# Kernel optimization log

Hardware: AMD Instinct MI355X
Metric: run time of the kernel (lower is better)

Reference implementation:

```python
import jax, jax.numpy as jnp
import numpy as np

B = 128      # graphs per side
N = 512      # nodes per graph (max for dense batch)
TOT = B * N  # 65536 total nodes per side
FIN = 128
F1, F2, F3 = 64, 64, 32
TN = 16      # tensor_neurons
BINS = 16
BN = 16      # bottleneck neurons
E = 16 * TOT # edges per side


def setup_inputs() -> dict:
    key = jax.random.key(0)
    ks = jax.random.split(key, 20)
    nrm = lambda k, shape, s=0.1: (jax.random.normal(k, shape, jnp.float32) * s)
    batch = jnp.repeat(jnp.arange(B, dtype=jnp.int32), N)
    return {
        'x1': jax.random.normal(ks[0], (TOT, FIN), jnp.float32),
        'x2': jax.random.normal(ks[1], (TOT, FIN), jnp.float32),
        'edge_index_1': jax.random.randint(ks[2], (2, E), 0, TOT, jnp.int32),
        'edge_index_2': jax.random.randint(ks[3], (2, E), 0, TOT, jnp.int32),
        'batch_1': batch,
        'batch_2': batch,
        'W1': nrm(ks[4], (FIN, F1)), 'b1': jnp.zeros((F1,), jnp.float32),
        'W2': nrm(ks[5], (F1, F2)), 'b2': jnp.zeros((F2,), jnp.float32),
        'W3': nrm(ks[6], (F2, F3)), 'b3': jnp.zeros((F3,), jnp.float32),
        'att_W': nrm(ks[7], (F3, F3)),
        'ntn_W': nrm(ks[8], (F3, F3, TN)),
        'ntn_V': nrm(ks[9], (TN, 2 * F3)),
        'ntn_b': jnp.zeros((TN,), jnp.float32),
        'fc1_W': nrm(ks[10], (TN + BINS, BN)),
        'fc1_b': jnp.zeros((BN,), jnp.float32),
        'sc_W': nrm(ks[11], (BN, 1)),
        'sc_b': jnp.zeros((1,), jnp.float32),
    }


def _gcn(x, W, b, src, dst):
    # PyG GCNConv: h = XW; add self-loops; D^{-1/2} A D^{-1/2} aggregation; + bias
    h = x @ W
    deg = jnp.zeros((TOT,), jnp.float32).at[dst].add(1.0) + 1.0  # incl. self-loop
    dis = jax.lax.rsqrt(deg)
    msg = h[src] * (dis[src] * dis[dst])[:, None]
    out = jnp.zeros_like(h).at[dst].add(msg) + h * (1.0 / deg)[:, None]
    return out + b


def _conv_pass(x, ei, W1, b1, W2, b2, W3, b3):
    # dropout is identity in eval mode
    h = jax.nn.relu(_gcn(x, W1, b1, ei[0], ei[1]))
    h = jax.nn.relu(_gcn(h, W2, b2, ei[0], ei[1]))
    return _gcn(h, W3, b3, ei[0], ei[1])


def _to_dense_batch(x, batch):
    ones = jnp.ones((TOT,), jnp.float32)
    cnt = jax.ops.segment_sum(ones, batch, num_segments=B)  # [B]
    starts = jnp.concatenate([jnp.zeros((1,), jnp.int32), jnp.cumsum(cnt.astype(jnp.int32))[:-1]])
    pos = jnp.arange(TOT, dtype=jnp.int32) - starts[batch]
    dense = jnp.zeros((B, N, x.shape[1]), x.dtype).at[batch, pos].set(x)
    cnt_i = cnt.astype(jnp.int32)
    return dense, cnt_i


def _histogram(af1, af2, batch_1, batch_2):
    d1, cnt1 = _to_dense_batch(af1, batch_1)
    d2, cnt2 = _to_dense_batch(af2, batch_2)
    nn = jnp.maximum(cnt1, cnt2)  # [B]
    sc = jax.nn.sigmoid(jax.lax.stop_gradient(jnp.einsum('bnf,bmf->bnm', d1, d2)))  # [B,N,N]
    ar = jnp.arange(N)
    valid = (ar[None, :, None] < nn[:, None, None]) & (ar[None, None, :] < nn[:, None, None])
    big = jnp.float32(1e30)
    mn = jnp.min(jnp.where(valid, sc, big), axis=(1, 2))
    mx = jnp.max(jnp.where(valid, sc, -big), axis=(1, 2))
    rng = jnp.where(mx > mn, mx - mn, jnp.float32(1.0))
    bidx = jnp.clip(jnp.floor((sc - mn[:, None, None]) / rng[:, None, None] * BINS), 0, BINS - 1).astype(jnp.int32)
    ids = jnp.arange(B, dtype=jnp.int32)[:, None, None] * BINS + bidx
    hist = jnp.zeros((B * BINS,), jnp.float32).at[ids.reshape(-1)].add(valid.reshape(-1).astype(jnp.float32))
    hist = hist.reshape(B, BINS)
    return hist / hist.sum(axis=1, keepdims=True)


def _att_pool(h, batch, att_W):
    cnt = jax.ops.segment_sum(jnp.ones((TOT,), jnp.float32), batch, num_segments=B)
    g = jax.ops.segment_sum(h @ att_W, batch, num_segments=B) / cnt[:, None]
    t = jnp.tanh(g)                                   # [B,F3] global context
    s = jax.nn.sigmoid(jnp.sum(h * t[batch], axis=1)) # [TOT] attention
    return jax.ops.segment_sum(h * s[:, None], batch, num_segments=B)


def reference(x1, x2, edge_index_1, edge_index_2, batch_1, batch_2,
              W1, b1, W2, b2, W3, b3, att_W, ntn_W, ntn_V, ntn_b,
              fc1_W, fc1_b, sc_W, sc_b):
    af1 = _conv_pass(x1, edge_index_1, W1, b1, W2, b2, W3, b3)
    af2 = _conv_pass(x2, edge_index_2, W1, b1, W2, b2, W3, b3)
    hist = _histogram(af1, af2, batch_1, batch_2)
    p1 = _att_pool(af1, batch_1, att_W)
    p2 = _att_pool(af2, batch_2, att_W)
    # Neural Tensor Network
    bilin = jnp.einsum('bi,ijk,bj->bk', p1, ntn_W, p2)
    blk = jnp.concatenate([p1, p2], axis=1) @ ntn_V.T
    scores = jax.nn.relu(bilin + blk + ntn_b)
    feat = jnp.concatenate([scores, hist], axis=1)
    h = jax.nn.relu(feat @ fc1_W + fc1_b)
    return jax.nn.sigmoid(h @ sc_W + sc_b).reshape(-1)
```

## Files before the change

### kernel.cpp

```cpp
#include <hip/hip_runtime.h>
#include <hip/hip_bf16.h>

constexpr int    TOT = 65536;
constexpr int    TOT2 = 131072;
constexpr long long Ec = 16LL * TOT;
constexpr int    NB  = 1024;
constexpr int    BKN = 128;
constexpr int    CAP = 2560;
constexpr int    NKEY = 1024;

typedef unsigned int   uint32;
typedef unsigned short ushort16;
typedef __attribute__((ext_vector_type(8))) short bf16x8;
typedef __attribute__((ext_vector_type(4))) float f32x4;

__device__ __forceinline__ float sigm(float x) { return 1.f / (1.f + __expf(-x)); }

__device__ __forceinline__ uint32 f2bf_rne(float x) {
    uint32 u = __float_as_uint(x);
    return (u + 0x7fffu + ((u >> 16) & 1u)) >> 16;
}
__device__ __forceinline__ float2 bf2f(uint32 u) {
    return make_float2(__uint_as_float(u << 16), __uint_as_float(u & 0xffff0000u));
}
__device__ __forceinline__ float bf1f(ushort16 u) {
    return __uint_as_float(((uint32)u) << 16);
}
__device__ __forceinline__ uint32 relu_bf2(uint32 v) {
    uint32 keep = (((int)v < 0) ? 0u : 0xFFFF0000u) | ((v & 0x8000u) ? 0u : 0x0000FFFFu);
    return v & keep;
}

__global__ void setup_k(const float* __restrict__ W1, const float* __restrict__ W2,
                        const float* __restrict__ W3, ushort16* __restrict__ Wt1,
                        ushort16* __restrict__ Wt2, ushort16* __restrict__ Wt3,
                        const int* __restrict__ b1, const int* __restrict__ b2,
                        int* __restrict__ cnt, int* __restrict__ st) {
    int t = blockIdx.x * 256 + threadIdx.x;
    if (t < 8192) {
        int j = t >> 7, k = t & 127;
        Wt1[t] = (ushort16)f2bf_rne(W1[k * 64 + j]);
    } else if (t < 12288) {
        int u = t - 8192; int j = u >> 6, k = u & 63;
        Wt2[u] = (ushort16)f2bf_rne(W2[k * 64 + j]);
    } else if (t < 14336) {
        int u = t - 12288; int j = u >> 6, k = u & 63;
        Wt3[u] = (ushort16)f2bf_rne(W3[k * 32 + j]);
    } else if (t < 14592) {
        int q = t - 14336;
        const int* bat = (q < 128) ? b1 : b2;
        const int g = q & 127;
        int lo = 0, hi = TOT;
        while (lo < hi) { int m = (lo + hi) >> 1; if (bat[m] < g) lo = m + 1; else hi = m; }
        const int s0 = lo;
        hi = TOT;
        while (lo < hi) { int m = (lo + hi) >> 1; if (bat[m] < g + 1) lo = m + 1; else hi = m; }
        st[q] = s0;
        cnt[q] = lo - s0;
    }
}

__global__ __launch_bounds__(256) void bktfill2_k(const int* __restrict__ ei1, const int* __restrict__ ei2,
                                                  int* __restrict__ gcnt, uint32* __restrict__ bkt) {
    __shared__ int hist[NB];
    __shared__ int hbase[NB];
    const int tid = threadIdx.x, blk = blockIdx.x;
#pragma unroll
    for (int q = 0; q < 4; ++q) hist[q * 256 + tid] = 0;
    __syncthreads();
    const long long base = (long long)blk * 8192;
    for (int q = 0; q < 32; ++q) {
        long long e = base + q * 256 + tid;
        int d = (e < Ec) ? ei1[Ec + e] : (TOT + ei2[Ec + (e - Ec)]);
        atomicAdd(&hist[d >> 7], 1);
    }
    __syncthreads();
#pragma unroll
    for (int q = 0; q < 4; ++q) {
        int bb = q * 256 + tid;
        int c = hist[bb];
        hbase[bb] = c ? atomicAdd(&gcnt[bb], c) : 0;
        hist[bb] = 0;
    }
    __syncthreads();
    for (int q = 0; q < 32; ++q) {
        long long e = base + q * 256 + tid;
        int s, d;
        if (e < Ec) { s = ei1[e]; d = ei1[Ec + e]; }
        else        { long long e2 = e - Ec; s = TOT + ei2[e2]; d = TOT + ei2[Ec + e2]; }
        int bb = d >> 7;
        int lofs = atomicAdd(&hist[bb], 1);
        bkt[(size_t)bb * CAP + hbase[bb] + lofs] = (uint32)s | ((uint32)(d & 127) << 20);
    }
}

__global__ __launch_bounds__(256) void bktsort_k(const int* __restrict__ gcnt, const uint32* __restrict__ bkt,
                                                 uint32* __restrict__ csr, int* __restrict__ rowstart,
                                                 int* __restrict__ rowend, float* __restrict__ dis) {
    __shared__ int keyc[NKEY];
    __shared__ int wsum[4];
    const int b = blockIdx.x, tid = threadIdx.x;
    const int ne = gcnt[b];
    const int e0 = b * CAP;
#pragma unroll
    for (int q = 0; q < 4; ++q) keyc[q * 256 + tid] = 0;
    __syncthreads();
    for (int i = tid; i < ne; i += 256) {
        uint32 v = bkt[e0 + i];
        int dl = v >> 20, src = v & 0x1FFFF;
        atomicAdd(&keyc[dl * 8 + ((src >> 13) & 7)], 1);
    }
    __syncthreads();
    const int lane = tid & 63, wid = tid >> 6;
    int s0 = keyc[tid * 4], s1 = keyc[tid * 4 + 1], s2 = keyc[tid * 4 + 2], s3 = keyc[tid * 4 + 3];
    int tot = s0 + s1 + s2 + s3;
    int inc = tot;
#pragma unroll
    for (int d = 1; d < 64; d <<= 1) { int n = __shfl_up(inc, d, 64); if (lane >= d) inc += n; }
    if (lane == 63) wsum[wid] = inc;
    __syncthreads();
    int wbase = 0;
    for (int q = 0; q < wid; ++q) wbase += wsum[q];
    const int myoff = wbase + inc - tot;
    __syncthreads();
    keyc[tid * 4]     = myoff;
    keyc[tid * 4 + 1] = myoff + s0;
    keyc[tid * 4 + 2] = myoff + s0 + s1;
    keyc[tid * 4 + 3] = myoff + s0 + s1 + s2;
    __syncthreads();
    if (tid < BKN) {
        int off_dl = keyc[tid * 8];
        int nxt = (tid < 127) ? keyc[(tid + 1) * 8] : ne;
        rowstart[b * BKN + tid] = e0 + off_dl;
        rowend[b * BKN + tid]   = e0 + nxt;
        dis[b * BKN + tid] = rsqrtf((float)(nxt - off_dl) + 1.0f);
    }
    __syncthreads();
    for (int i = tid; i < ne; i += 256) {
        uint32 v = bkt[e0 + i];
        int dl = v >> 20, src = v & 0x1FFFF;
        int pos = atomicAdd(&keyc[dl * 8 + ((src >> 13) & 7)], 1);
        csr[e0 + pos] = (uint32)src;
    }
}

template<int K, int NC, bool RELU, bool XBF>
__global__ __launch_bounds__(256) void gemmf_k(const void* __restrict__ X1v,
                                               const void* __restrict__ X2v,
                                               const ushort16* __restrict__ Wt,
                                               const float* __restrict__ dis,
                                               ushort16* __restrict__ out) {
    constexpr int NK = K / 32;
    const int tid = threadIdx.x, lane = tid & 63, wave = tid >> 6;
    const int i0 = (blockIdx.x * 4 + wave) * 16;
    const int arow = i0 + (lane & 15);
    const int ks0 = (lane >> 4) * 8;
    bf16x8 a[NK];
    if (XBF) {
        const uint32* Xr = (arow < TOT) ? (const uint32*)X1v + (size_t)arow * (K / 2)
                                        : (const uint32*)X2v + (size_t)(arow - TOT) * (K / 2);
#pragma unroll
        for (int s = 0; s < NK; ++s) {
            uint4 v = *(const uint4*)(Xr + s * 16 + ks0 / 2);
            if (RELU) { v.x = relu_bf2(v.x); v.y = relu_bf2(v.y); v.z = relu_bf2(v.z); v.w = relu_bf2(v.w); }
            a[s] = *(bf16x8*)&v;
        }
    } else {
        const float* Xr = (arow < TOT) ? (const float*)X1v + (size_t)arow * K
                                       : (const float*)X2v + (size_t)(arow - TOT) * K;
#pragma unroll
        for (int s = 0; s < NK; ++s) {
            float4 v0 = *(const float4*)(Xr + s * 32 + ks0);
            float4 v1 = *(const float4*)(Xr + s * 32 + ks0 + 4);
            if (RELU) {
                v0.x = fmaxf(v0.x, 0.f); v0.y = fmaxf(v0.y, 0.f); v0.z = fmaxf(v0.z, 0.f); v0.w = fmaxf(v0.w, 0.f);
                v1.x = fmaxf(v1.x, 0.f); v1.y = fmaxf(v1.y, 0.f); v1.z = fmaxf(v1.z, 0.f); v1.w = fmaxf(v1.w, 0.f);
            }
            uint4 p;
            p.x = f2bf_rne(v0.x) | (f2bf_rne(v0.y) << 16);
            p.y = f2bf_rne(v0.z) | (f2bf_rne(v0.w) << 16);
            p.z = f2bf_rne(v1.x) | (f2bf_rne(v1.y) << 16);
            p.w = f2bf_rne(v1.z) | (f2bf_rne(v1.w) << 16);
            a[s] = *(bf16x8*)&p;
        }
    }
    float dv[4];
#pragma unroll
    for (int r = 0; r < 4; ++r) dv[r] = dis[i0 + (lane >> 4) * 4 + r];
#pragma unroll
    for (int jt = 0; jt < NC / 16; ++jt) {
        const int col = jt * 16 + (lane & 15);
        f32x4 cc = {0.f, 0.f, 0.f, 0.f};
#pragma unroll
        for (int s = 0; s < NK; ++s) {
            bf16x8 b = *(const bf16x8*)(Wt + (size_t)col * K + s * 32 + ks0);
            cc = __builtin_amdgcn_mfma_f32_16x16x32_bf16(a[s], b, cc, 0, 0, 0);
        }
#pragma unroll
        for (int r = 0; r < 4; ++r) {
            const int row = i0 + (lane >> 4) * 4 + r;
            out[(size_t)row * NC + col] = (ushort16)f2bf_rne(cc[r] * dv[r]);
        }
    }
}

template<int NC>
__global__ __launch_bounds__(256) void gatherb_k(uint32* __restrict__ out, const uint32* __restrict__ hs,
                                                 const float* __restrict__ dis, const float* __restrict__ bias,
                                                 const int* __restrict__ rowstart, const int* __restrict__ rowend,
                                                 const uint32* __restrict__ csr) {
    constexpr int TPN = NC / 2;
    constexpr int NG  = 256 / TPN;
    constexpr int NPB = 2 * NG;
    int bid;
    {
        const int xcd = blockIdx.x & 7, idx = blockIdx.x >> 3;
        const int half = gridDim.x >> 1;
        bid = (xcd < 4) ? (idx * 4 + xcd) : (half + idx * 4 + (xcd - 4));
    }
    const int tid = threadIdx.x;
    const int cp = tid & (TPN - 1);
    const int g = tid / TPN;
    const int nodeA = bid * NPB + g;
    const int nodeB = nodeA + NG;
    const float2 bb = ((const float2*)bias)[cp];
    float2 svA = bf2f(hs[(size_t)nodeA * TPN + cp]);
    float2 svB = bf2f(hs[(size_t)nodeB * TPN + cp]);
    float a0 = svA.x, a1 = svA.y;
    float b0 = svB.x, b1 = svB.y;
    int eA = rowstart[nodeA]; const int eA1 = rowend[nodeA];
    int eB = rowstart[nodeB]; const int eB1 = rowend[nodeB];
    while (true) {
        const bool ca = (eA + 8 <= eA1), cb = (eB + 8 <= eB1);
        if (!ca && !cb) break;
        uint32 pa[8], pb[8];
        if (ca) {
#pragma unroll
            for (int q = 0; q < 8; ++q) pa[q] = hs[(size_t)csr[eA + q] * TPN + cp];
        }
        if (cb) {
#pragma unroll
            for (int q = 0; q < 8; ++q) pb[q] = hs[(size_t)csr[eB + q] * TPN + cp];
        }
        if (ca) {
#pragma unroll
            for (int q = 0; q < 8; ++q) { float2 f = bf2f(pa[q]); a0 += f.x; a1 += f.y; }
            eA += 8;
        }
        if (cb) {
#pragma unroll
            for (int q = 0; q < 8; ++q) { float2 f = bf2f(pb[q]); b0 += f.x; b1 += f.y; }
            eB += 8;
        }
    }
    if (eA + 4 <= eA1) {
        uint32 p[4];
#pragma unroll
        for (int q = 0; q < 4; ++q) p[q] = hs[(size_t)csr[eA + q] * TPN + cp];
#pragma unroll
        for (int q = 0; q < 4; ++q) { float2 f = bf2f(p[q]); a0 += f.x; a1 += f.y; }
        eA += 4;
    }
    for (; eA < eA1; ++eA) { float2 f = bf2f(hs[(size_t)csr[eA] * TPN + cp]); a0 += f.x; a1 += f.y; }
    if (eB + 4 <= eB1) {
        uint32 p[4];
#pragma unroll
        for (int q = 0; q < 4; ++q) p[q] = hs[(size_t)csr[eB + q] * TPN + cp];
#pragma unroll
        for (int q = 0; q < 4; ++q) { float2 f = bf2f(p[q]); b0 += f.x; b1 += f.y; }
        eB += 4;
    }
    for (; eB < eB1; ++eB) { float2 f = bf2f(hs[(size_t)csr[eB] * TPN + cp]); b0 += f.x; b1 += f.y; }
    const float dvA = dis[nodeA], dvB = dis[nodeB];
    out[(size_t)nodeA * TPN + cp] = f2bf_rne(a0 * dvA + bb.x) | (f2bf_rne(a1 * dvA + bb.y) << 16);
    out[(size_t)nodeB * TPN + cp] = f2bf_rne(b0 * dvB + bb.x) | (f2bf_rne(b1 * dvB + bb.y) << 16);
}

__global__ __launch_bounds__(256) void attpool_k(const ushort16* __restrict__ af,
                                                 const int* __restrict__ cnt, const int* __restrict__ st,
                                                 const float* __restrict__ attW, float* __restrict__ pool) {
    const int side = blockIdx.x >> 7, b = blockIdx.x & 127;
    const ushort16* h = af + (size_t)side * TOT * 32;
    const int c = cnt[side * 128 + b], s0 = st[side * 128 + b];
    const int f = threadIdx.x & 31, grp = threadIdx.x >> 5;
    __shared__ float red[8][32];
    __shared__ float mhS[32], tS[32];
    float acc = 0.f;
    for (int i = grp; i < c; i += 8) acc += bf1f(h[(size_t)(s0 + i) * 32 + f]);
    red[grp][f] = acc;
    __syncthreads();
    if (threadIdx.x < 32) { float tt = 0; for (int g = 0; g < 8; ++g) tt += red[g][f]; mhS[f] = tt / (float)c; }
    __syncthreads();
    if (threadIdx.x < 32) {
        float g = 0;
        for (int k = 0; k < 32; ++k) g += mhS[k] * attW[k * 32 + f];
        tS[f] = tanhf(g);
    }
    __syncthreads();
    const float tf = tS[f];
    acc = 0.f;
    for (int i = grp; i < c; i += 8) {
        float hv = bf1f(h[(size_t)(s0 + i) * 32 + f]);
        float pr = hv * tf;
#pragma unroll
        for (int m = 16; m; m >>= 1) pr += __shfl_xor(pr, m, 32);
        float sA = 1.f / (1.f + expf(-pr));
        acc += hv * sA;
    }
    __syncthreads();
    red[grp][f] = acc;
    __syncthreads();
    if (threadIdx.x < 32) {
        float tt = 0; for (int g = 0; g < 8; ++g) tt += red[g][f];
        pool[(size_t)(side * 128 + b) * 32 + f] = tt;
    }
}

__global__ __launch_bounds__(256) void mm2_k(const ushort16* __restrict__ afb,
                                             const int* __restrict__ cnt, const int* __restrict__ st,
                                             float* __restrict__ bmn, float* __restrict__ bmx) {
    const int b = blockIdx.x >> 3, it8 = blockIdx.x & 7;
    const int c1 = cnt[b], c2 = cnt[128 + b];
    const int s1 = st[b], s2 = st[128 + b];
    const int nn = max(c1, c2);
    const int tid = threadIdx.x, lane = tid & 63, wave = tid >> 6;
    const int itile = it8 * 4 + wave;
    const int i0 = itile * 16;
    float lmn = 1e30f, lmx = -1e30f;
    if (i0 < nn) {
        const int arow = i0 + (lane & 15);
        const int koff = (lane >> 4) * 8;
        bf16x8 a = {0, 0, 0, 0, 0, 0, 0, 0};
        if (arow < c1) a = *(const bf16x8*)(afb + (size_t)(s1 + arow) * 32 + koff);
        const int ibase = i0 + (lane >> 4) * 4;
        const int njt = (nn + 15) >> 4;
        for (int jt = 0; jt < njt; ++jt) {
            const int brow = jt * 16 + (lane & 15);
            bf16x8 bb = {0, 0, 0, 0, 0, 0, 0, 0};
            if (brow < c2) bb = *(const bf16x8*)(afb + (size_t)(s2 + brow) * 32 + koff);
            f32x4 cc = {0.f, 0.f, 0.f, 0.f};
            cc = __builtin_amdgcn_mfma_f32_16x16x32_bf16(a, bb, cc, 0, 0, 0);
            if (brow < nn) {
#pragma unroll
                for (int r = 0; r < 4; ++r) {
                    if (ibase + r < nn) { lmn = fminf(lmn, cc[r]); lmx = fmaxf(lmx, cc[r]); }
                }
            }
        }
    }
    __shared__ float redn[256], redx[256];
    redn[tid] = lmn; redx[tid] = lmx;
    __syncthreads();
    for (int sr = 128; sr; sr >>= 1) {
        if (tid < sr) {
            redn[tid] = fminf(redn[tid], redn[tid + sr]);
            redx[tid] = fmaxf(redx[tid], redx[tid + sr]);
        }
        __syncthreads();
    }
    if (tid == 0) { bmn[blockIdx.x] = redn[0]; bmx[blockIdx.x] = redx[0]; }
}

__global__ __launch_bounds__(256) void bin2_k(const ushort16* __restrict__ afb,
                                              const int* __restrict__ cnt, const int* __restrict__ st,
                                              const float* __restrict__ bmn, const float* __restrict__ bmx,
                                              float* __restrict__ hist) {
    const int b = blockIdx.x >> 3, it8 = blockIdx.x & 7;
    const int c1 = cnt[b], c2 = cnt[128 + b];
    const int s1 = st[b], s2 = st[128 + b];
    const int nn = max(c1, c2);
    const int tid = threadIdx.x, lane = tid & 63, wave = tid >> 6;
    const int itile = it8 * 4 + wave;
    const int i0 = itile * 16;
    float dmn = 1e30f, dmx = -1e30f;
#pragma unroll
    for (int q = 0; q < 8; ++q) {
        dmn = fminf(dmn, bmn[(b << 3) + q]);
        dmx = fmaxf(dmx, bmx[(b << 3) + q]);
    }
    const float vMn = sigm(dmn), vMx = sigm(dmx);
    const float vScale = 16.f / ((vMx > vMn) ? (vMx - vMn) : 1.f);
    __shared__ int hloc[16 * 256];
    __shared__ int part[64];
#pragma unroll
    for (int q = 0; q < 16; ++q) hloc[q * 256 + tid] = 0;
    __syncthreads();
    if (i0 < nn) {
        const int arow = i0 + (lane & 15);
        const int koff = (lane >> 4) * 8;
        bf16x8 a = {0, 0, 0, 0, 0, 0, 0, 0};
        if (arow < c1) a = *(const bf16x8*)(afb + (size_t)(s1 + arow) * 32 + koff);
        const int ibase = i0 + (lane >> 4) * 4;
        const int njt = (nn + 15) >> 4;
        for (int jt = 0; jt < njt; ++jt) {
            const int brow = jt * 16 + (lane & 15);
            bf16x8 bb = {0, 0, 0, 0, 0, 0, 0, 0};
            if (brow < c2) bb = *(const bf16x8*)(afb + (size_t)(s2 + brow) * 32 + koff);
            f32x4 cc = {0.f, 0.f, 0.f, 0.f};
            cc = __builtin_amdgcn_mfma_f32_16x16x32_bf16(a, bb, cc, 0, 0, 0);
            if (brow < nn) {
#pragma unroll
                for (int r = 0; r < 4; ++r) {
                    if (ibase + r < nn) {
                        float t = (sigm(cc[r]) - vMn) * vScale;
                        int bi = (int)floorf(t);
                        bi = bi < 0 ? 0 : (bi > 15 ? 15 : bi);
                        hloc[bi * 256 + tid] += 1;
                    }
                }
            }
        }
    }
    __syncthreads();
    if (tid < 64) {
        const int bin = tid & 15, q = tid >> 4;
        int s = 0;
        for (int t2 = q * 64; t2 < q * 64 + 64; ++t2) s += hloc[bin * 256 + t2];
        part[tid] = s;
    }
    __syncthreads();
    if (tid < 16) {
        int s = part[tid] + part[16 + tid] + part[32 + tid] + part[48 + tid];
        atomicAdd(&hist[b * 16 + tid], (float)s);
    }
}

__global__ __launch_bounds__(64) void final_k(const float* __restrict__ pool, const float* __restrict__ hist,
                                              const int* __restrict__ cnt,
                                              const float* __restrict__ ntnW, const float* __restrict__ ntnV,
                                              const float* __restrict__ ntnb, const float* __restrict__ fc1W,
                                              const float* __restrict__ fc1b, const float* __restrict__ scW,
                                              const float* __restrict__ scb, float* __restrict__ out) {
    const int b = blockIdx.x;
    const int tid = threadIdx.x;
    __shared__ float P1[32], P2[32], feat[32], red[64];
    if (tid < 32) { P1[tid] = pool[b * 32 + tid]; P2[tid] = pool[4096 + b * 32 + tid]; }
    __syncthreads();
    const int k = tid & 15, part = tid >> 4;
    float acc = 0.f;
    for (int i = part * 8; i < part * 8 + 8; ++i) {
        float p1i = P1[i];
        for (int j = 0; j < 32; ++j) acc += p1i * P2[j] * ntnW[(i * 32 + j) * 16 + k];
    }
    red[tid] = acc;
    __syncthreads();
    if (tid < 16) {
        float bl = red[tid] + red[16 + tid] + red[32 + tid] + red[48 + tid];
        float blk = ntnb[tid];
        for (int i = 0; i < 32; ++i) blk += P1[i] * ntnV[tid * 64 + i];
        for (int j = 0; j < 32; ++j) blk += P2[j] * ntnV[tid * 64 + 32 + j];
        feat[tid] = fmaxf(bl + blk, 0.f);
        const int nn = max(cnt[b], cnt[128 + b]);
        feat[16 + tid] = hist[b * 16 + tid] / (float)(nn * nn);
    }
    __syncthreads();
    if (tid < 16) {
        float h = fc1b[tid];
        for (int f = 0; f < 32; ++f) h += feat[f] * fc1W[f * 16 + tid];
        red[tid] = fmaxf(h, 0.f);
    }
    __syncthreads();
    if (tid == 0) {
        float o = scb[0];
        for (int j = 0; j < 16; ++j) o += red[j] * scW[j];
        out[b] = 1.f / (1.f + expf(-o));
    }
}

extern "C" void kernel_launch(void* const* d_in, const int* in_sizes, int n_in,
                              void* d_out, int out_size, void* d_ws, size_t ws_size,
                              hipStream_t stream) {
    const float* x1   = (const float*)d_in[0];
    const float* x2   = (const float*)d_in[1];
    const int*   ei1  = (const int*)d_in[2];
    const int*   ei2  = (const int*)d_in[3];
    const int*   bat1 = (const int*)d_in[4];
    const int*   bat2 = (const int*)d_in[5];
    const float* W1   = (const float*)d_in[6];
    const float* b1   = (const float*)d_in[7];
    const float* W2   = (const float*)d_in[8];
    const float* b2   = (const float*)d_in[9];
    const float* W3   = (const float*)d_in[10];
    const float* b3   = (const float*)d_in[11];
    const float* attW = (const float*)d_in[12];
    const float* ntnW = (const float*)d_in[13];
    const float* ntnV = (const float*)d_in[14];
    const float* ntnb = (const float*)d_in[15];
    const float* fc1W = (const float*)d_in[16];
    const float* fc1b = (const float*)d_in[17];
    const float* scW  = (const float*)d_in[18];
    const float* scb  = (const float*)d_in[19];
    float* out = (float*)d_out;

    uint32* Hbuf   = (uint32*)d_ws;
    uint32* Gb     = Hbuf + (size_t)TOT2 * 32;
    uint32* AFb    = Gb + (size_t)TOT2 * 32;
    uint32* bkt    = AFb + (size_t)TOT2 * 16;
    uint32* csr    = bkt + (size_t)NB * CAP;
    float* dis     = (float*)(csr + (size_t)NB * CAP);
    int*   rowstart= (int*)(dis + TOT2);
    int*   rowend  = rowstart + TOT2;
    int*   gcnt    = rowend + TOT2;
    int*   cnt     = gcnt + NB;
    int*   st      = cnt + 256;
    float* pool    = (float*)(st + 256);
    float* hist    = pool + 8192;
    float* bmn     = hist + 2048;
    float* bmx     = bmn + 1024;
    ushort16* Wt1  = (ushort16*)(bmx + 1024);
    ushort16* Wt2  = Wt1 + 8192;
    ushort16* Wt3  = Wt2 + 4096;

    hipMemsetAsync(gcnt, 0, NB * sizeof(int), stream);
    hipMemsetAsync(hist, 0, 2048 * sizeof(float), stream);
    setup_k<<<57, 256, 0, stream>>>(W1, W2, W3, Wt1, Wt2, Wt3, bat1, bat2, cnt, st);
    bktfill2_k<<<256, 256, 0, stream>>>(ei1, ei2, gcnt, bkt);
    bktsort_k<<<NB, 256, 0, stream>>>(gcnt, bkt, csr, rowstart, rowend, dis);

    gemmf_k<128, 64, false, false><<<2048, 256, 0, stream>>>(x1, x2, Wt1, dis, (ushort16*)Hbuf);
    gatherb_k<64><<<TOT2 / 16, 256, 0, stream>>>(Gb, Hbuf, dis, b1, rowstart, rowend, csr);

    gemmf_k<64, 64, true, true><<<2048, 256, 0, stream>>>(Gb, Gb, Wt2, dis, (ushort16*)Hbuf);
    gatherb_k<64><<<TOT2 / 16, 256, 0, stream>>>(Gb, Hbuf, dis, b2, rowstart, rowend, csr);

    gemmf_k<64, 32, true, true><<<2048, 256, 0, stream>>>(Gb, Gb, Wt3, dis, (ushort16*)Hbuf);
    gatherb_k<32><<<TOT2 / 32, 256, 0, stream>>>(AFb, Hbuf, dis, b3, rowstart, rowend, csr);

    attpool_k<<<256, 256, 0, stream>>>((const ushort16*)AFb, cnt, st, attW, pool);
    mm2_k<<<1024, 256, 0, stream>>>((const ushort16*)AFb, cnt, st, bmn, bmx);
    bin2_k<<<1024, 256, 0, stream>>>((const ushort16*)AFb, cnt, st, bmn, bmx, hist);
    final_k<<<128, 64, 0, stream>>>(pool, hist, cnt, ntnW, ntnV, ntnb, fc1W, fc1b, scW, scb, out);
}
```

Measured before the change: 329.2 us.

## Pad CSR rows to 4-aligned offsets for vector index loads, simplify bucket sort

The bucket sort now counts only per-destination degree and pads each row's start to a multiple of four. This lets the gather kernels read neighbour indices with 16-byte vector loads instead of scalar loads. It drops the source-locality sub-key sort, so gathers may lose some cache locality, and CAP grows to hold the padding. It also folds the two memsets into the setup kernel and spreads the bucket fill over 8x more blocks.

```diff
diff --git a/kernel.cpp b/kernel.cpp
--- a/kernel.cpp
+++ b/kernel.cpp
@@ -6,8 +6,7 @@
 constexpr long long Ec = 16LL * TOT;
 constexpr int    NB  = 1024;
 constexpr int    BKN = 128;
-constexpr int    CAP = 2560;
-constexpr int    NKEY = 1024;
+constexpr int    CAP = 2816;
 
 typedef unsigned int   uint32;
 typedef unsigned short ushort16;
@@ -35,7 +34,8 @@
                         const float* __restrict__ W3, ushort16* __restrict__ Wt1,
                         ushort16* __restrict__ Wt2, ushort16* __restrict__ Wt3,
                         const int* __restrict__ b1, const int* __restrict__ b2,
-                        int* __restrict__ cnt, int* __restrict__ st) {
+                        int* __restrict__ cnt, int* __restrict__ st,
+                        int* __restrict__ gcnt, float* __restrict__ hist) {
     int t = blockIdx.x * 256 + threadIdx.x;
     if (t < 8192) {
         int j = t >> 7, k = t & 127;
@@ -57,6 +57,10 @@
         while (lo < hi) { int m = (lo + hi) >> 1; if (bat[m] < g + 1) lo = m + 1; else hi = m; }
         st[q] = s0;
         cnt[q] = lo - s0;
+    } else if (t < 15616) {
+        gcnt[t - 14592] = 0;
+    } else if (t < 17664) {
+        hist[t - 15616] = 0.f;
     }
 }
 
@@ -68,8 +72,9 @@
 #pragma unroll
     for (int q = 0; q < 4; ++q) hist[q * 256 + tid] = 0;
     __syncthreads();
-    const long long base = (long long)blk * 8192;
-    for (int q = 0; q < 32; ++q) {
+    const long long base = (long long)blk * 1024;
+#pragma unroll
+    for (int q = 0; q < 4; ++q) {
         long long e = base + q * 256 + tid;
         int d = (e < Ec) ? ei1[Ec + e] : (TOT + ei2[Ec + (e - Ec)]);
         atomicAdd(&hist[d >> 7], 1);
@@ -83,7 +88,8 @@
         hist[bb] = 0;
     }
     __syncthreads();
-    for (int q = 0; q < 32; ++q) {
+#pragma unroll
+    for (int q = 0; q < 4; ++q) {
         long long e = base + q * 256 + tid;
         int s, d;
         if (e < Ec) { s = ei1[e]; d = ei1[Ec + e]; }
@@ -97,50 +103,33 @@
 __global__ __launch_bounds__(256) void bktsort_k(const int* __restrict__ gcnt, const uint32* __restrict__ bkt,
                                                  uint32* __restrict__ csr, int* __restrict__ rowstart,
                                                  int* __restrict__ rowend, float* __restrict__ dis) {
-    __shared__ int keyc[NKEY];
-    __shared__ int wsum[4];
+    __shared__ int deg[BKN], offs[BKN], cur[BKN];
     const int b = blockIdx.x, tid = threadIdx.x;
     const int ne = gcnt[b];
     const int e0 = b * CAP;
-#pragma unroll
-    for (int q = 0; q < 4; ++q) keyc[q * 256 + tid] = 0;
+    if (tid < BKN) deg[tid] = 0;
+    __syncthreads();
+    for (int i = tid; i < ne; i += 256) atomicAdd(&deg[bkt[e0 + i] >> 20], 1);
+    __syncthreads();
+    if (tid == 0) {
+        int o = 0;
+        for (int q = 0; q < BKN; ++q) {
+            int al = (o + 3) & ~3;
+            offs[q] = al; cur[q] = al; o = al + deg[q];
+        }
+    }
+    __syncthreads();
+    if (tid < BKN) {
+        rowstart[b * BKN + tid] = e0 + offs[tid];
+        rowend[b * BKN + tid]   = e0 + offs[tid] + deg[tid];
+        dis[b * BKN + tid] = rsqrtf((float)deg[tid] + 1.0f);
+    }
     __syncthreads();
     for (int i = tid; i < ne; i += 256) {
         uint32 v = bkt[e0 + i];
-        int dl = v >> 20, src = v & 0x1FFFF;
-        atomicAdd(&keyc[dl * 8 + ((src >> 13) & 7)], 1);
-    }
-    __syncthreads();
-    const int lane = tid & 63, wid = tid >> 6;
-    int s0 = keyc[tid * 4], s1 = keyc[tid * 4 + 1], s2 = keyc[tid * 4 + 2], s3 = keyc[tid * 4 + 3];
-    int tot = s0 + s1 + s2 + s3;
-    int inc = tot;
-#pragma unroll
-    for (int d = 1; d < 64; d <<= 1) { int n = __shfl_up(inc, d, 64); if (lane >= d) inc += n; }
-    if (lane == 63) wsum[wid] = inc;
-    __syncthreads();
-    int wbase = 0;
-    for (int q = 0; q < wid; ++q) wbase += wsum[q];
-    const int myoff = wbase + inc - tot;
-    __syncthreads();
-    keyc[tid * 4]     = myoff;
-    keyc[tid * 4 + 1] = myoff + s0;
-    keyc[tid * 4 + 2] = myoff + s0 + s1;
-    keyc[tid * 4 + 3] = myoff + s0 + s1 + s2;
-    __syncthreads();
-    if (tid < BKN) {
-        int off_dl = keyc[tid * 8];
-        int nxt = (tid < 127) ? keyc[(tid + 1) * 8] : ne;
-        rowstart[b * BKN + tid] = e0 + off_dl;
-        rowend[b * BKN + tid]   = e0 + nxt;
-        dis[b * BKN + tid] = rsqrtf((float)(nxt - off_dl) + 1.0f);
-    }
-    __syncthreads();
-    for (int i = tid; i < ne; i += 256) {
-        uint32 v = bkt[e0 + i];
-        int dl = v >> 20, src = v & 0x1FFFF;
-        int pos = atomicAdd(&keyc[dl * 8 + ((src >> 13) & 7)], 1);
-        csr[e0 + pos] = (uint32)src;
+        int dl = v >> 20;
+        int pos = atomicAdd(&cur[dl], 1);
+        csr[e0 + pos] = v & 0x1FFFF;
     }
 }
 
@@ -233,14 +222,21 @@
     while (true) {
         const bool ca = (eA + 8 <= eA1), cb = (eB + 8 <= eB1);
         if (!ca && !cb) break;
+        uint4 ia0, ia1, ib0, ib1;
+        if (ca) { ia0 = *(const uint4*)&csr[eA]; ia1 = *(const uint4*)&csr[eA + 4]; }
+        if (cb) { ib0 = *(const uint4*)&csr[eB]; ib1 = *(const uint4*)&csr[eB + 4]; }
         uint32 pa[8], pb[8];
         if (ca) {
-#pragma unroll
-            for (int q = 0; q < 8; ++q) pa[q] = hs[(size_t)csr[eA + q] * TPN + cp];
+            pa[0] = hs[(size_t)ia0.x * TPN + cp]; pa[1] = hs[(size_t)ia0.y * TPN + cp];
+            pa[2] = hs[(size_t)ia0.z * TPN + cp]; pa[3] = hs[(size_t)ia0.w * TPN + cp];
+            pa[4] = hs[(size_t)ia1.x * TPN + cp]; pa[5] = hs[(size_t)ia1.y * TPN + cp];
+            pa[6] = hs[(size_t)ia1.z * TPN + cp]; pa[7] = hs[(size_t)ia1.w * TPN + cp];
         }
         if (cb) {
-#pragma unroll
-            for (int q = 0; q < 8; ++q) pb[q] = hs[(size_t)csr[eB + q] * TPN + cp];
+            pb[0] = hs[(size_t)ib0.x * TPN + cp]; pb[1] = hs[(size_t)ib0.y * TPN + cp];
+            pb[2] = hs[(size_t)ib0.z * TPN + cp]; pb[3] = hs[(size_t)ib0.w * TPN + cp];
+            pb[4] = hs[(size_t)ib1.x * TPN + cp]; pb[5] = hs[(size_t)ib1.y * TPN + cp];
+            pb[6] = hs[(size_t)ib1.z * TPN + cp]; pb[7] = hs[(size_t)ib1.w * TPN + cp];
         }
         if (ca) {
 #pragma unroll
@@ -254,18 +250,18 @@
         }
     }
     if (eA + 4 <= eA1) {
-        uint32 p[4];
-#pragma unroll
-        for (int q = 0; q < 4; ++q) p[q] = hs[(size_t)csr[eA + q] * TPN + cp];
+        uint4 i4 = *(const uint4*)&csr[eA];
+        uint32 p[4] = { hs[(size_t)i4.x * TPN + cp], hs[(size_t)i4.y * TPN + cp],
+                        hs[(size_t)i4.z * TPN + cp], hs[(size_t)i4.w * TPN + cp] };
 #pragma unroll
         for (int q = 0; q < 4; ++q) { float2 f = bf2f(p[q]); a0 += f.x; a1 += f.y; }
         eA += 4;
     }
     for (; eA < eA1; ++eA) { float2 f = bf2f(hs[(size_t)csr[eA] * TPN + cp]); a0 += f.x; a1 += f.y; }
     if (eB + 4 <= eB1) {
-        uint32 p[4];
-#pragma unroll
-        for (int q = 0; q < 4; ++q) p[q] = hs[(size_t)csr[eB + q] * TPN + cp];
+        uint4 i4 = *(const uint4*)&csr[eB];
+        uint32 p[4] = { hs[(size_t)i4.x * TPN + cp], hs[(size_t)i4.y * TPN + cp],
+                        hs[(size_t)i4.z * TPN + cp], hs[(size_t)i4.w * TPN + cp] };
 #pragma unroll
         for (int q = 0; q < 4; ++q) { float2 f = bf2f(p[q]); b0 += f.x; b1 += f.y; }
         eB += 4;
@@ -511,10 +507,8 @@
     ushort16* Wt2  = Wt1 + 8192;
     ushort16* Wt3  = Wt2 + 4096;
 
-    hipMemsetAsync(gcnt, 0, NB * sizeof(int), stream);
-    hipMemsetAsync(hist, 0, 2048 * sizeof(float), stream);
-    setup_k<<<57, 256, 0, stream>>>(W1, W2, W3, Wt1, Wt2, Wt3, bat1, bat2, cnt, st);
-    bktfill2_k<<<256, 256, 0, stream>>>(ei1, ei2, gcnt, bkt);
+    setup_k<<<69, 256, 0, stream>>>(W1, W2, W3, Wt1, Wt2, Wt3, bat1, bat2, cnt, st, gcnt, hist);
+    bktfill2_k<<<2048, 256, 0, stream>>>(ei1, ei2, gcnt, bkt);
     bktsort_k<<<NB, 256, 0, stream>>>(gcnt, bkt, csr, rowstart, rowend, dis);
 
     gemmf_k<128, 64, false, false><<<2048, 256, 0, stream>>>(x1, x2, Wt1, dis, (ushort16*)Hbuf);
```

Measured after the change: 366.2 us. 11.3% more time.
